# Kernel tuning notes

Measured on AMD Instinct MI355X. Metric: run time of the kernel, lower is better.

Reference implementation:

```python
import jax, jax.numpy as jnp
import numpy as np

ALPHA = 0.5
B = 4096
K = 8192


def setup_inputs() -> dict:
    key = jax.random.key(0)
    k1, k2 = jax.random.split(key)
    outputs = jax.random.normal(k1, (B, K), dtype=jnp.float32)
    labels = jax.random.randint(k2, (B,), 0, K)
    targets = jax.nn.one_hot(labels, K, dtype=jnp.float32)
    S = jnp.eye(K, dtype=jnp.float32)          # soft-label matrix (state)
    S_t = jnp.zeros((K, K), dtype=jnp.float32)  # running stats (state)
    count = jnp.zeros((K, 1), dtype=jnp.float32)
    return {"outputs": outputs, "targets": targets, "S": S, "S_t": S_t, "count": count}


def reference(outputs, targets, S, S_t, count):
    # loss path
    ls = jax.nn.log_softmax(outputs, axis=1)          # [B, K]
    bsz = outputs.shape[0]
    target_label = jnp.argmax(targets, axis=1)        # [B]
    prediction = jnp.argmax(outputs, axis=1)          # [B]
    soft_targets = S[target_label]                    # [B, K] gather
    ce_hard = -(ls * targets).sum() / bsz
    ce_soft = -(ls * soft_targets).sum() / bsz
    loss = ALPHA * ce_hard + (1.0 - ALPHA) * ce_soft

    # stats accumulation (the original python for-loop, as one fused scatter-add)
    probs = jax.nn.softmax(jax.lax.stop_gradient(outputs), axis=1)  # [B, K]
    correct = (prediction == target_label).astype(probs.dtype)      # [B]
    S_t_new = S_t + jax.ops.segment_sum(probs * correct[:, None], target_label, num_segments=K)
    count_new = count + jax.ops.segment_sum(correct, target_label, num_segments=K)[:, None]
    return loss, S_t_new, count_new
```

## Files before the change

### kernel.cpp

```cpp
#include <hip/hip_runtime.h>
#include <math.h>

#define K 8192
#define BROWS 4096
#define ALPHA 0.5f

__device__ __forceinline__ void argmax_combine(float& v, int& i, float v2, int i2){
  if (v2 > v || (v2 == v && i2 < i)) { v = v2; i = i2; }
}

__global__ __launch_bounds__(256) void fused_kernel(
    const float* __restrict__ outputs,
    const float* __restrict__ targets,
    const float* __restrict__ S,
    const float* __restrict__ S_t,
    float* __restrict__ out_St,
    float* __restrict__ rowloss,
    int*   __restrict__ rowtl,
    int*   __restrict__ rowcorrect,
    float* __restrict__ rowm,
    float* __restrict__ rowinvZ)
{
  const int bb = blockIdx.x;
  const int t  = threadIdx.x;
  const int r  = bb % 3;

  if (r != 0){
    const int c = (bb / 3) * 2 + (r - 1);
    size_t base = (size_t)c * 8192 + t;
#pragma unroll
    for (int j = 0; j < 32; ++j)
      out_St[base + (size_t)j*256] = S_t[base + (size_t)j*256];
    return;
  }

  const int b = bb / 3;
  const int lane = t & 63;
  const int wid  = t >> 6;

  const float4* orow = (const float4*)(outputs + (size_t)b * K);
  float x[32];
#pragma unroll
  for (int i = 0; i < 8; ++i){
    float4 v = orow[i*256 + t];
    x[4*i+0]=v.x; x[4*i+1]=v.y; x[4*i+2]=v.z; x[4*i+3]=v.w;
  }

  float mv = -INFINITY; int mi = 0x7fffffff;
#pragma unroll
  for (int i = 0; i < 8; ++i){
#pragma unroll
    for (int c = 0; c < 4; ++c){
      int idx = i*1024 + t*4 + c;
      argmax_combine(mv, mi, x[4*i+c], idx);
    }
  }

  const float4* trow = (const float4*)(targets + (size_t)b * K);
  float tv = -INFINITY; int ti = 0x7fffffff;
  float d_hard = 0.f, s_hard = 0.f;
#pragma unroll
  for (int i = 0; i < 8; ++i){
    float4 v = trow[i*256 + t];
    float tc[4] = {v.x, v.y, v.z, v.w};
#pragma unroll
    for (int c = 0; c < 4; ++c){
      int idx = i*1024 + t*4 + c;
      d_hard += x[4*i+c] * tc[c];
      s_hard += tc[c];
      argmax_combine(tv, ti, tc[c], idx);
    }
  }

#pragma unroll
  for (int off = 32; off; off >>= 1){
    float v2 = __shfl_down(mv, off, 64); int i2 = __shfl_down(mi, off, 64);
    argmax_combine(mv, mi, v2, i2);
    v2 = __shfl_down(tv, off, 64); i2 = __shfl_down(ti, off, 64);
    argmax_combine(tv, ti, v2, i2);
  }

  __shared__ float s_v[2][4]; __shared__ int s_i[2][4];
  __shared__ float s_m; __shared__ int s_pred; __shared__ int s_tl;
  if (lane == 0){ s_v[0][wid]=mv; s_i[0][wid]=mi; s_v[1][wid]=tv; s_i[1][wid]=ti; }
  __syncthreads();
  if (t == 0){
    float av=s_v[0][0]; int ai=s_i[0][0];
    float bv=s_v[1][0]; int bi=s_i[1][0];
#pragma unroll
    for (int w=1; w<4; ++w){
      argmax_combine(av, ai, s_v[0][w], s_i[0][w]);
      argmax_combine(bv, bi, s_v[1][w], s_i[1][w]);
    }
    s_m = av; s_pred = ai; s_tl = bi;
  }
  __syncthreads();
  const float m  = s_m;
  const int   tl = s_tl;

  float se = 0.f;
#pragma unroll
  for (int i = 0; i < 32; ++i) se += expf(x[i] - m);

  const float4* srow = (const float4*)(S + (size_t)tl * K);
  float d_soft = 0.f, s_soft = 0.f;
#pragma unroll
  for (int i = 0; i < 8; ++i){
    float4 v = srow[i*256 + t];
    d_soft += x[4*i+0]*v.x + x[4*i+1]*v.y + x[4*i+2]*v.z + x[4*i+3]*v.w;
    s_soft += v.x + v.y + v.z + v.w;
  }

  float sums[5] = {d_hard, s_hard, se, d_soft, s_soft};
#pragma unroll
  for (int off = 32; off; off >>= 1){
#pragma unroll
    for (int j = 0; j < 5; ++j) sums[j] += __shfl_down(sums[j], off, 64);
  }
  __shared__ float s_sums[4][5];
  if (lane == 0){
#pragma unroll
    for (int j = 0; j < 5; ++j) s_sums[wid][j] = sums[j];
  }
  __syncthreads();
  if (t == 0){
    float tot[5];
#pragma unroll
    for (int j=0;j<5;++j)
      tot[j] = s_sums[0][j]+s_sums[1][j]+s_sums[2][j]+s_sums[3][j];
    float Z = tot[2];
    float logZ = logf(Z);
    float ceh = -(tot[0] - (m + logZ) * tot[1]);
    float ces = -(tot[3] - (m + logZ) * tot[4]);
    rowloss[b]    = (ALPHA * ceh + (1.0f - ALPHA) * ces) * (1.0f / (float)BROWS);
    rowtl[b]      = tl;
    rowcorrect[b] = (s_pred == tl) ? 1 : 0;
    rowm[b]       = m;
    rowinvZ[b]    = 1.0f / Z;
  }
}

__global__ __launch_bounds__(256) void tail_kernel(const float* __restrict__ outputs,
    const int* __restrict__ rowtl, const int* __restrict__ rowcorrect,
    const float* __restrict__ rowm, const float* __restrict__ rowinvZ,
    const float* __restrict__ rowloss, const float* __restrict__ count,
    float* __restrict__ out_loss, float* __restrict__ out_St,
    float* __restrict__ out_count){
  const int b = blockIdx.x;
  const int t = threadIdx.x;
  if (b == BROWS){
    float s = 0.f;
    for (int i = t; i < BROWS; i += 256) s += rowloss[i];
#pragma unroll
    for (int off = 32; off; off >>= 1) s += __shfl_down(s, off, 64);
    __shared__ float sh[4];
    if ((t & 63) == 0) sh[t >> 6] = s;
    __syncthreads();
    if (t == 0) out_loss[0] = sh[0] + sh[1] + sh[2] + sh[3];
    for (int i = t; i < K; i += 256) out_count[i] = count[i];
    return;
  }
  if (!rowcorrect[b]) return;
  const int tl = rowtl[b];
  const float m = rowm[b], invZ = rowinvZ[b];
  const float* orow = outputs + (size_t)b * K;
  float* drow = out_St + (size_t)tl * K;
  for (int k = t; k < K; k += 256)
    atomicAdd(&drow[k], expf(orow[k] - m) * invZ);
  if (t == 0) atomicAdd(&out_count[tl], 1.0f);
}

extern "C" void kernel_launch(void* const* d_in, const int* in_sizes, int n_in,
                              void* d_out, int out_size, void* d_ws, size_t ws_size,
                              hipStream_t stream) {
  const float* outputs = (const float*)d_in[0];
  const float* targets = (const float*)d_in[1];
  const float* S       = (const float*)d_in[2];
  const float* S_t     = (const float*)d_in[3];
  const float* count   = (const float*)d_in[4];

  float* out       = (float*)d_out;
  float* out_loss  = out;
  float* out_St    = out + 1;
  float* out_count = out + 1 + (size_t)K * K;

  float* rowloss    = (float*)d_ws;
  float* rowm       = rowloss + BROWS;
  float* rowinvZ    = rowm + BROWS;
  int*   rowtl      = (int*)(rowinvZ + BROWS);
  int*   rowcorrect = rowtl + BROWS;

  hipLaunchKernelGGL(fused_kernel, dim3(3 * BROWS), dim3(256), 0, stream,
                     outputs, targets, S, S_t, out_St,
                     rowloss, rowtl, rowcorrect, rowm, rowinvZ);
  hipLaunchKernelGGL(tail_kernel, dim3(BROWS + 1), dim3(256), 0, stream,
                     outputs, rowtl, rowcorrect, rowm, rowinvZ, rowloss, count,
                     out_loss, out_St, out_count);
}
```

Baseline: 727.1 us.

## Split S_t copy into dedicated aligned float4 kernel and stage row in LDS

Moves the 256MB S_t to out_St copy out of the fused row kernel into its own kernel. The new kernel offsets by three floats so destination stores are 16-byte aligned float4 writes, since out_St sits one float into the output buffer, and handles the leftover elements separately. The row kernel now batches its global loads up front and stashes the outputs row in shared memory, fusing the exp-sum into the soft-target loop to cut register pressure. This adds a third kernel launch and serialises the copy after the row-stats work instead of interleaving the two.

New measurement: 744.3 us. 1.02x slower.

```diff
diff --git a/kernel.cpp b/kernel.cpp
--- a/kernel.cpp
+++ b/kernel.cpp
@@ -5,70 +5,64 @@
 #define BROWS 4096
 #define ALPHA 0.5f
 
+typedef float f4u __attribute__((ext_vector_type(4), aligned(4)));
+
 __device__ __forceinline__ void argmax_combine(float& v, int& i, float v2, int i2){
   if (v2 > v || (v2 == v && i2 < i)) { v = v2; i = i2; }
 }
 
-__global__ __launch_bounds__(256) void fused_kernel(
+__global__ __launch_bounds__(256) void row_stats_kernel(
     const float* __restrict__ outputs,
     const float* __restrict__ targets,
     const float* __restrict__ S,
-    const float* __restrict__ S_t,
-    float* __restrict__ out_St,
     float* __restrict__ rowloss,
     int*   __restrict__ rowtl,
     int*   __restrict__ rowcorrect,
     float* __restrict__ rowm,
     float* __restrict__ rowinvZ)
 {
-  const int bb = blockIdx.x;
-  const int t  = threadIdx.x;
-  const int r  = bb % 3;
-
-  if (r != 0){
-    const int c = (bb / 3) * 2 + (r - 1);
-    size_t base = (size_t)c * 8192 + t;
-#pragma unroll
-    for (int j = 0; j < 32; ++j)
-      out_St[base + (size_t)j*256] = S_t[base + (size_t)j*256];
-    return;
-  }
-
-  const int b = bb / 3;
+  __shared__ float xs[K];
+  __shared__ float s_v[2][4]; __shared__ int s_i[2][4];
+  __shared__ float s_m; __shared__ int s_pred; __shared__ int s_tl;
+  __shared__ float s_sums[4][5];
+
+  const int b = blockIdx.x;
+  const int t = threadIdx.x;
   const int lane = t & 63;
   const int wid  = t >> 6;
+  float4* xs4 = (float4*)xs;
 
   const float4* orow = (const float4*)(outputs + (size_t)b * K);
-  float x[32];
+  float4 xv[8];
+#pragma unroll
+  for (int i = 0; i < 8; ++i) xv[i] = orow[i*256 + t];
+
+  float mv = -INFINITY; int mi = 0x7fffffff;
 #pragma unroll
   for (int i = 0; i < 8; ++i){
-    float4 v = orow[i*256 + t];
-    x[4*i+0]=v.x; x[4*i+1]=v.y; x[4*i+2]=v.z; x[4*i+3]=v.w;
-  }
-
-  float mv = -INFINITY; int mi = 0x7fffffff;
-#pragma unroll
-  for (int i = 0; i < 8; ++i){
-#pragma unroll
-    for (int c = 0; c < 4; ++c){
-      int idx = i*1024 + t*4 + c;
-      argmax_combine(mv, mi, x[4*i+c], idx);
-    }
+    xs4[i*256 + t] = xv[i];
+    const float xc[4] = {xv[i].x, xv[i].y, xv[i].z, xv[i].w};
+#pragma unroll
+    for (int c = 0; c < 4; ++c)
+      argmax_combine(mv, mi, xc[c], i*1024 + t*4 + c);
   }
 
   const float4* trow = (const float4*)(targets + (size_t)b * K);
+  float4 tvv[8];
+#pragma unroll
+  for (int i = 0; i < 8; ++i) tvv[i] = trow[i*256 + t];
+
   float tv = -INFINITY; int ti = 0x7fffffff;
   float d_hard = 0.f, s_hard = 0.f;
 #pragma unroll
   for (int i = 0; i < 8; ++i){
-    float4 v = trow[i*256 + t];
-    float tc[4] = {v.x, v.y, v.z, v.w};
+    const float xc[4] = {xv[i].x, xv[i].y, xv[i].z, xv[i].w};
+    const float tc[4] = {tvv[i].x, tvv[i].y, tvv[i].z, tvv[i].w};
 #pragma unroll
     for (int c = 0; c < 4; ++c){
-      int idx = i*1024 + t*4 + c;
-      d_hard += x[4*i+c] * tc[c];
+      d_hard += xc[c] * tc[c];
       s_hard += tc[c];
-      argmax_combine(tv, ti, tc[c], idx);
+      argmax_combine(tv, ti, tc[c], i*1024 + t*4 + c);
     }
   }
 
@@ -79,9 +73,6 @@
     v2 = __shfl_down(tv, off, 64); i2 = __shfl_down(ti, off, 64);
     argmax_combine(tv, ti, v2, i2);
   }
-
-  __shared__ float s_v[2][4]; __shared__ int s_i[2][4];
-  __shared__ float s_m; __shared__ int s_pred; __shared__ int s_tl;
   if (lane == 0){ s_v[0][wid]=mv; s_i[0][wid]=mi; s_v[1][wid]=tv; s_i[1][wid]=ti; }
   __syncthreads();
   if (t == 0){
@@ -98,17 +89,23 @@
   const float m  = s_m;
   const int   tl = s_tl;
 
-  float se = 0.f;
-#pragma unroll
-  for (int i = 0; i < 32; ++i) se += expf(x[i] - m);
-
   const float4* srow = (const float4*)(S + (size_t)tl * K);
-  float d_soft = 0.f, s_soft = 0.f;
+  float4 svv[8];
+#pragma unroll
+  for (int i = 0; i < 8; ++i) svv[i] = srow[i*256 + t];
+
+  float se = 0.f, d_soft = 0.f, s_soft = 0.f;
 #pragma unroll
   for (int i = 0; i < 8; ++i){
-    float4 v = srow[i*256 + t];
-    d_soft += x[4*i+0]*v.x + x[4*i+1]*v.y + x[4*i+2]*v.z + x[4*i+3]*v.w;
-    s_soft += v.x + v.y + v.z + v.w;
+    float4 xr = xs4[i*256 + t];
+    const float xc[4] = {xr.x, xr.y, xr.z, xr.w};
+    const float sc[4] = {svv[i].x, svv[i].y, svv[i].z, svv[i].w};
+#pragma unroll
+    for (int c = 0; c < 4; ++c){
+      se     += expf(xc[c] - m);
+      d_soft += xc[c] * sc[c];
+      s_soft += sc[c];
+    }
   }
 
   float sums[5] = {d_hard, s_hard, se, d_soft, s_soft};
@@ -117,7 +114,6 @@
 #pragma unroll
     for (int j = 0; j < 5; ++j) sums[j] += __shfl_down(sums[j], off, 64);
   }
-  __shared__ float s_sums[4][5];
   if (lane == 0){
 #pragma unroll
     for (int j = 0; j < 5; ++j) s_sums[wid][j] = sums[j];
@@ -140,6 +136,39 @@
   }
 }
 
+__global__ __launch_bounds__(256) void copy_st_kernel(const float* __restrict__ src,
+                                                      float* __restrict__ dst){
+  const f4u*  s4 = (const f4u*)(src + 3);
+  float4*     d4 = (float4*)(dst + 3);
+  const size_t n4     = 16777215UL;
+  const size_t stride = 2097152UL;
+  const size_t i = (size_t)blockIdx.x * 256 + threadIdx.x;
+
+  if (i != stride - 1){
+    float4 v[8];
+#pragma unroll
+    for (int k = 0; k < 8; ++k){
+      f4u u = s4[i + (size_t)k * stride];
+      v[k] = *(const float4*)&u;
+    }
+#pragma unroll
+    for (int k = 0; k < 8; ++k)
+      d4[i + (size_t)k * stride] = v[k];
+  } else {
+    float4 v[7];
+#pragma unroll
+    for (int k = 0; k < 7; ++k){
+      f4u u = s4[i + (size_t)k * stride];
+      v[k] = *(const float4*)&u;
+    }
+#pragma unroll
+    for (int k = 0; k < 7; ++k)
+      d4[i + (size_t)k * stride] = v[k];
+    dst[0] = src[0]; dst[1] = src[1]; dst[2] = src[2];
+    dst[67108863] = src[67108863];
+  }
+}
+
 __global__ __launch_bounds__(256) void tail_kernel(const float* __restrict__ outputs,
     const int* __restrict__ rowtl, const int* __restrict__ rowcorrect,
     const float* __restrict__ rowm, const float* __restrict__ rowinvZ,
@@ -190,9 +219,9 @@
   int*   rowtl      = (int*)(rowinvZ + BROWS);
   int*   rowcorrect = rowtl + BROWS;
 
-  hipLaunchKernelGGL(fused_kernel, dim3(3 * BROWS), dim3(256), 0, stream,
-                     outputs, targets, S, S_t, out_St,
-                     rowloss, rowtl, rowcorrect, rowm, rowinvZ);
+  hipLaunchKernelGGL(row_stats_kernel, dim3(BROWS), dim3(256), 0, stream,
+                     outputs, targets, S, rowloss, rowtl, rowcorrect, rowm, rowinvZ);
+  hipLaunchKernelGGL(copy_st_kernel, dim3(8192), dim3(256), 0, stream, S_t, out_St);
   hipLaunchKernelGGL(tail_kernel, dim3(BROWS + 1), dim3(256), 0, stream,
                      outputs, rowtl, rowcorrect, rowm, rowinvZ, rowloss, count,
                      out_loss, out_St, out_count);
```
